# Performance work log

Measured on AMD Instinct MI355X. Metric: run time of the kernel, lower is better.

Reference implementation:

```python
import jax, jax.numpy as jnp
from jax import lax
import numpy as np

DG = 8          # deformable_groups
NF = 64         # num_feat
K = 3
KK = K * K


def conv3(x, w, b):
    # 3x3 'same' conv, NCHW / OIHW
    return lax.conv_general_dilated(x, w, (1, 1), 'SAME',
                                    dimension_numbers=('NCHW', 'OIHW', 'NCHW')) + b[None, :, None, None]


def deform_conv(x, offset, w, b, dg=DG):
    # Offset-only deformable conv (DCN), 3x3, stride 1, pad 1.
    # x: (B,C,H,W); offset: (B, dg*KK*2, H, W) ordered (group, kernel_pos, [dy,dx])
    B, C, H, W = x.shape
    Cg = C // dg
    dt = x.dtype
    off = offset.reshape(B, dg, KK, 2, H, W)
    gy = jnp.arange(H, dtype=dt)[:, None]                      # (H,1)
    gx = jnp.arange(W, dtype=dt)[None, :]                      # (1,W)
    ky = (jnp.arange(KK) // K - 1).astype(dt)[:, None, None]   # (KK,1,1)
    kx = (jnp.arange(KK) % K - 1).astype(dt)[:, None, None]
    py = gy + ky + off[:, :, :, 0]                             # (B,dg,KK,H,W)
    px = gx + kx + off[:, :, :, 1]
    xg = x.reshape(B, dg, Cg, H, W)

    def sample(img, py, px):
        # img (Cg,H,W); py,px (KK,H,W) -> (Cg,KK,H,W); zero padding outside image
        y0 = jnp.floor(py); x0 = jnp.floor(px)
        wy = py - y0; wx = px - x0
        y0 = y0.astype(jnp.int32); x0 = x0.astype(jnp.int32)
        imf = img.reshape(Cg, H * W)

        def gather(yi, xi):
            valid = ((yi >= 0) & (yi < H) & (xi >= 0) & (xi < W)).astype(dt)
            flat = (jnp.clip(yi, 0, H - 1) * W + jnp.clip(xi, 0, W - 1)).reshape(-1)
            return imf[:, flat].reshape(Cg, KK, H, W) * valid

        v00 = gather(y0, x0);     v01 = gather(y0, x0 + 1)
        v10 = gather(y0 + 1, x0); v11 = gather(y0 + 1, x0 + 1)
        return (v00 * (1 - wy) * (1 - wx) + v01 * (1 - wy) * wx
                + v10 * wy * (1 - wx) + v11 * wy * wx)

    samp = jax.vmap(jax.vmap(sample))(xg, py, px)   # (B,dg,Cg,KK,H,W)
    wr = w.reshape(-1, dg, Cg, KK)                  # (Cout,dg,Cg,KK) from (Cout,Cin,3,3)
    out = jnp.einsum('bgckhw,ogck->bohw', samp, wr)
    return out + b[None, :, None, None]


def _forward(pf, xc, cr_w, cr_b, off1_w, off1_b, dc1_w, dc1_b, off2_w, off2_b,
             dc2_w, dc2_b, off3_w, off3_b, dc3_w, dc3_b, off4_w, off4_b,
             dc4_w, dc4_b, rec_w, rec_b):
    B, N, C, H, W = pf.shape
    center = N // 2
    ref = pf[:, center]
    ys = []
    for i in range(N):  # N is a small static frame count (5)
        if i == center:
            ys.append(xc[:, None])
            continue
        supp = pf[:, i]
        fea = conv3(jnp.concatenate([ref, supp], axis=1), cr_w, cr_b)
        fea = deform_conv(fea, conv3(fea, off1_w, off1_b), dc1_w, dc1_b)
        fea = deform_conv(fea, conv3(fea, off2_w, off2_b), dc2_w, dc2_b)
        fea = deform_conv(supp, conv3(fea, off3_w, off3_b), dc3_w, dc3_b)
        aligned = deform_conv(fea, conv3(fea, off4_w, off4_b), dc4_w, dc4_b)
        ys.append(conv3(aligned, rec_w, rec_b)[:, None])
    return jnp.concatenate(ys, axis=1)  # (B, N, 3, H, W)


def setup_inputs() -> dict:
    key = jax.random.key(0)
    ks = jax.random.split(key, 16)
    B, N, C, H, W = 2, 5, NF, 128, 128
    offc = 18 * DG

    def cw(k, cout, cin):
        # matches init_weights: normal(0, sqrt(2 / (k*k*out_channels)))
        return jax.random.normal(k, (cout, cin, 3, 3), jnp.float32) * float(np.sqrt(2.0 / (9 * cout)))

    return {
        'precomputed_features': jax.random.normal(ks[0], (B, N, C, H, W), jnp.float32),
        'x_center': jax.random.normal(ks[1], (B, 3, H, W), jnp.float32),
        'cr_w': cw(ks[2], C, 2 * C), 'cr_b': jnp.zeros((C,), jnp.float32),
        'off1_w': cw(ks[3], offc, C), 'off1_b': jnp.zeros((offc,), jnp.float32),
        'dc1_w': cw(ks[4], C, C), 'dc1_b': jnp.zeros((C,), jnp.float32),
        'off2_w': cw(ks[5], offc, C), 'off2_b': jnp.zeros((offc,), jnp.float32),
        'dc2_w': cw(ks[6], C, C), 'dc2_b': jnp.zeros((C,), jnp.float32),
        'off3_w': cw(ks[7], offc, C), 'off3_b': jnp.zeros((offc,), jnp.float32),
        'dc3_w': cw(ks[8], C, C), 'dc3_b': jnp.zeros((C,), jnp.float32),
        'off4_w': cw(ks[9], offc, C), 'off4_b': jnp.zeros((offc,), jnp.float32),
        'dc4_w': cw(ks[10], C, C), 'dc4_b': jnp.zeros((C,), jnp.float32),
        'rec_w': cw(ks[11], 3, C), 'rec_b': jnp.zeros((3,), jnp.float32),
    }


def reference(precomputed_features, x_center, cr_w, cr_b, off1_w, off1_b, dc1_w, dc1_b,
              off2_w, off2_b, dc2_w, dc2_b, off3_w, off3_b, dc3_w, dc3_b,
              off4_w, off4_b, dc4_w, dc4_b, rec_w, rec_b):
    return _forward(precomputed_features, x_center, cr_w, cr_b, off1_w, off1_b, dc1_w, dc1_b,
                    off2_w, off2_b, dc2_w, dc2_b, off3_w, off3_b, dc3_w, dc3_b,
                    off4_w, off4_b, dc4_w, dc4_b, rec_w, rec_b)
```

## Files before the change

kernel.cpp:

```cpp
#include <hip/hip_runtime.h>

#define HH 128
#define WW 128
#define HWP (HH*WW)
#define NC 64
#define NB 2
#define NN 5
#define OFFC 144
#define NKC 18

typedef __attribute__((ext_vector_type(8))) _Float16 half8;
typedef __attribute__((ext_vector_type(4))) float floatx4;
typedef __attribute__((ext_vector_type(2))) float floatx2;

__global__ __launch_bounds__(256) void copy_center_k(const float* __restrict__ xc,
                                                     float* __restrict__ out) {
    int idx = blockIdx.x * 256 + threadIdx.x;
    const int total = NB * 3 * HWP;
    if (idx >= total) return;
    int b = idx / (3 * HWP);
    int r = idx - b * 3 * HWP;
    out[(size_t)((b * NN + 2) * 3) * HWP + r] = xc[idx];
}

__global__ __launch_bounds__(256) void repack_k(const float* __restrict__ pf,
                                                float* __restrict__ dst, int job0, int is_ref)
{
    __shared__ float T[64][65];
    const int jl = blockIdx.y;
    const float* src;
    if (is_ref) {
        src = pf + (size_t)((jl * NN + 2) * NC) * HWP;
    } else {
        int jg = job0 + jl;
        int b = jg & 1, fi = jg >> 1;
        int frame = fi + (fi >= 2 ? 1 : 0);
        src = pf + (size_t)((b * NN + frame) * NC) * HWP;
    }
    float* d = dst + (size_t)jl * NC * HWP;
    const int p0 = blockIdx.x * 64;
    const int tid = threadIdx.x;
    const int lx = tid & 63, cg4 = tid >> 6;
#pragma unroll
    for (int cc = 0; cc < 16; ++cc) {
        int c = cc * 4 + cg4;
        T[c][lx] = src[(size_t)c * HWP + p0 + lx];
    }
    __syncthreads();
    const int px = tid >> 2, c0 = (tid & 3) * 16;
#pragma unroll
    for (int j = 0; j < 4; ++j) {
        floatx4 v = { T[c0 + j*4 + 0][px], T[c0 + j*4 + 1][px],
                      T[c0 + j*4 + 2][px], T[c0 + j*4 + 3][px] };
        *(floatx4*)(d + (size_t)(p0 + px) * 64 + c0 + j*4) = v;
    }
}

__global__ __launch_bounds__(256) void prew_k(const float* __restrict__ w,
                                              _Float16* __restrict__ wp,
                                              int nct, int nkc, int mode,
                                              int ci_off, int cin_src)
{
    int idx = blockIdx.x * 256 + threadIdx.x;
    if (idx >= nct * nkc * 64) return;
    int lane = idx & 63;
    int kc = (idx >> 6) % nkc;
    int ct = (idx >> 6) / nkc;
    int m = lane & 15, quad = lane >> 4;
    int co = ct * 16 + m;
    union { half8 v; _Float16 e[8]; } ph, pl;
#pragma unroll
    for (int j = 0; j < 8; ++j) {
        int k = kc * 32 + quad * 8 + j;
        float f = 0.f;
        if (mode == 0) {
            int kk = k >> 6, ci = k & 63;
            f = w[((size_t)co * cin_src + ci_off + ci) * 9 + kk];
        } else {
            int r = k / 160, kr = k - r * 160;
            if (kr < 144) {
                int g = r * 2 + kr / 72;
                int rr = kr % 72;
                int kk = rr >> 3, cg = rr & 7;
                f = w[((size_t)co * cin_src + g * 8 + cg) * 9 + kk];
            }
        }
        _Float16 h = (_Float16)f;
        ph.e[j] = h; pl.e[j] = (_Float16)(f - (float)h);
    }
    size_t base = (size_t)((ct * nkc + kc) * 2) * 512;
    *(half8*)(wp + base + lane * 8) = ph.v;
    *(half8*)(wp + base + 512 + lane * 8) = pl.v;
}

template<int NCT, int SRCMODE, int ADD>
__global__ __launch_bounds__(256, 3) void mconv_k(
    const float* __restrict__ src, const float* __restrict__ R,
    const float* __restrict__ S, const _Float16* __restrict__ wp,
    const float* __restrict__ bias, float* __restrict__ out, int job0)
{
    constexpr int PL = 1456;
    constexpr int Ct = NCT * 16;
    const int jl = blockIdx.y, jg = job0 + jl;
    const int b = jg & 1;
    const int tile = blockIdx.x;
    const int ty0 = (tile >> 3) << 3, tx0 = (tile & 7) << 4;
    const int tid = threadIdx.x;
    const int lane = tid & 63;
    const int wq = __builtin_amdgcn_readfirstlane(tid >> 6);
    const int n = lane & 15, quad = lane >> 4;

    const float* s0;
    if (SRCMODE == 0)      s0 = src + (size_t)jl * NC * HWP;
    else if (SRCMODE == 1) s0 = R + (size_t)b * NC * HWP;
    else                   s0 = S + (size_t)jl * NC * HWP;

    __shared__ _Float16 hh[8 * PL];
    __shared__ _Float16 ll[8 * PL];

    for (int t = tid; t < 360; t += 256) {
        int px = t >> 1, hf = t & 1;
        int hy = px / 18, hx = px - hy * 18;
        int gy = ty0 - 1 + hy, gx = tx0 - 1 + hx;
        bool ok = (gy >= 0 && gy < HH && gx >= 0 && gx < WW);
        const float* sp = s0 + (ok ? ((size_t)(gy * WW + gx) * 64) : 0) + hf * 32;
        int lb = px * 8;
#pragma unroll
        for (int c = 0; c < 4; ++c) {
            int cb = hf * 4 + c;
            floatx4 f0 = {0.f,0.f,0.f,0.f}, f1 = {0.f,0.f,0.f,0.f};
            if (ok) {
                f0 = *(const floatx4*)(sp + c * 8);
                f1 = *(const floatx4*)(sp + c * 8 + 4);
            }
            union { half8 v; _Float16 e[8]; } ph, pl;
#pragma unroll
            for (int j = 0; j < 4; ++j) {
                _Float16 h0 = (_Float16)f0[j], h1 = (_Float16)f1[j];
                ph.e[j] = h0;     ph.e[j+4] = h1;
                pl.e[j] = (_Float16)(f0[j] - (float)h0);
                pl.e[j+4] = (_Float16)(f1[j] - (float)h1);
            }
            *(half8*)&hh[cb * PL + lb] = ph.v;
            *(half8*)&ll[cb * PL + lb] = pl.v;
        }
    }
    __syncthreads();

    floatx4 acc0[NCT], acc1[NCT];
#pragma unroll
    for (int ct = 0; ct < NCT; ++ct) {
        acc0[ct] = floatx4{0.f, 0.f, 0.f, 0.f};
        acc1[ct] = floatx4{0.f, 0.f, 0.f, 0.f};
    }
    const int y0 = wq * 2, y1 = y0 + 1;
#pragma unroll
    for (int kc = 0; kc < NKC; ++kc) {
        const int kk = kc >> 1;
        const int dy = kk / 3, dx = kk % 3;
        const int cb = ((kc & 1) << 2) + quad;
        const int ix0 = cb * PL + ((y0 + dy) * 18 + n + dx) * 8;
        const int ix1 = cb * PL + ((y1 + dy) * 18 + n + dx) * 8;
        half8 B0h = *(const half8*)&hh[ix0];
        half8 B0l = *(const half8*)&ll[ix0];
        half8 B1h = *(const half8*)&hh[ix1];
        half8 B1l = *(const half8*)&ll[ix1];
        const _Float16* wk = wp + (size_t)kc * 1024 + lane * 8;
#pragma unroll
        for (int ct = 0; ct < NCT; ++ct) {
            const _Float16* wc = wk + (size_t)ct * NKC * 1024;
            half8 Ah = *(const half8*)wc;
            half8 Al = *(const half8*)(wc + 512);
            acc0[ct] = __builtin_amdgcn_mfma_f32_16x16x32_f16(Ah, B0h, acc0[ct], 0, 0, 0);
            acc0[ct] = __builtin_amdgcn_mfma_f32_16x16x32_f16(Ah, B0l, acc0[ct], 0, 0, 0);
            acc0[ct] = __builtin_amdgcn_mfma_f32_16x16x32_f16(Al, B0h, acc0[ct], 0, 0, 0);
            acc1[ct] = __builtin_amdgcn_mfma_f32_16x16x32_f16(Ah, B1h, acc1[ct], 0, 0, 0);
            acc1[ct] = __builtin_amdgcn_mfma_f32_16x16x32_f16(Ah, B1l, acc1[ct], 0, 0, 0);
            acc1[ct] = __builtin_amdgcn_mfma_f32_16x16x32_f16(Al, B1h, acc1[ct], 0, 0, 0);
        }
    }

    const int oy0 = ty0 + y0, oy1 = ty0 + y1, ox = tx0 + n;
#pragma unroll
    for (int ct = 0; ct < NCT; ++ct) {
        const floatx4 b4 = *(const floatx4*)(bias + ct * 16 + quad * 4);
        float* op0 = out + ((size_t)jl * HWP + (size_t)oy0 * WW + ox) * Ct
                         + ct * 16 + quad * 4;
        float* op1 = out + ((size_t)jl * HWP + (size_t)oy1 * WW + ox) * Ct
                         + ct * 16 + quad * 4;
        floatx4 v0 = acc0[ct], v1 = acc1[ct];
        if (ADD) {
            v0 += *(const floatx4*)op0;
            v1 += *(const floatx4*)op1;
        } else {
            v0 += b4;
            v1 += b4;
        }
        *(floatx4*)op0 = v0;
        *(floatx4*)op1 = v1;
    }
}

__global__ __launch_bounds__(256, 4) void mdeform_k(
    const float* __restrict__ in, const float* __restrict__ off,
    const _Float16* __restrict__ wp, const float* __restrict__ bias,
    float* __restrict__ out, int supp_mode, const float* __restrict__ S)
{
    constexpr int SROW = 166;
    const int jl = blockIdx.y;
    const int tile = blockIdx.x;
    const int ty0 = (tile >> 4) << 3, tx0 = (tile & 15) << 3;
    const int tid = threadIdx.x;
    const int lane = tid & 63;
    const int q = __builtin_amdgcn_readfirstlane(tid >> 6);
    const int n = lane & 15, quad = lane >> 4;

    const float* ibase = supp_mode ? (S + (size_t)jl * NC * HWP)
                                   : (in + (size_t)jl * NC * HWP);
    const float* obase = off + (size_t)jl * OFFC * HWP;

    __shared__ _Float16 sh[64 * SROW];
    __shared__ _Float16 sl[64 * SROW];

    for (int e = tid; e < 64 * 16; e += 256) {
        int row = e >> 4, col = 144 + (e & 15);
        sh[row * SROW + col] = (_Float16)0.f;
        sl[row * SROW + col] = (_Float16)0.f;
    }

    floatx4 acc[4];
#pragma unroll
    for (int s = 0; s < 4; ++s) acc[s] = floatx4{0.f, 0.f, 0.f, 0.f};

    for (int r = 0; r < 4; ++r) {
        __syncthreads();
        for (int i = 0; i < 9; ++i) {
            int idx = tid + (i << 8);
            int hf = idx & 1;
            int pair = idx >> 1;
            int gl = pair / 576;
            int rem = pair - gl * 576;
            int kk = rem >> 6;
            int px = rem & 63;
            int g = r * 2 + gl;
            int yy = ty0 + (px >> 3), xx = tx0 + (px & 7);
            floatx2 o2 = *(const floatx2*)(obase + (size_t)(yy * WW + xx) * OFFC
                                           + (g * 9 + kk) * 2);
            float pyf = (float)(yy + (kk / 3) - 1) + o2[0];
            float pxf = (float)(xx + (kk % 3) - 1) + o2[1];
            float fy = floorf(pyf), fx = floorf(pxf);
            float wy = pyf - fy, wx = pxf - fx;
            int y0 = (int)fy, x0 = (int)fx;
            int y1 = y0 + 1, x1 = x0 + 1;
            float m00 = (y0 >= 0 && y0 < HH && x0 >= 0 && x0 < WW) ? 1.f : 0.f;
            float m01 = (y0 >= 0 && y0 < HH && x1 >= 0 && x1 < WW) ? 1.f : 0.f;
            float m10 = (y1 >= 0 && y1 < HH && x0 >= 0 && x0 < WW) ? 1.f : 0.f;
            float m11 = (y1 >= 0 && y1 < HH && x1 >= 0 && x1 < WW) ? 1.f : 0.f;
            float w00 = (1.f - wy) * (1.f - wx) * m00;
            float w01 = (1.f - wy) * wx * m01;
            float w10 = wy * (1.f - wx) * m10;
            float w11 = wy * wx * m11;
            int cy0 = min(max(y0, 0), HH - 1), cy1 = min(max(y1, 0), HH - 1);
            int cx0 = min(max(x0, 0), WW - 1), cx1 = min(max(x1, 0), WW - 1);
            const int co = g * 8 + hf * 4;
            const float* p00 = ibase + (size_t)(cy0 * WW + cx0) * 64 + co;
            const float* p01 = ibase + (size_t)(cy0 * WW + cx1) * 64 + co;
            const float* p10 = ibase + (size_t)(cy1 * WW + cx0) * 64 + co;
            const float* p11 = ibase + (size_t)(cy1 * WW + cx1) * 64 + co;
            floatx4 a = *(const floatx4*)p00;
            floatx4 b = *(const floatx4*)p01;
            floatx4 c = *(const floatx4*)p10;
            floatx4 d = *(const floatx4*)p11;
            floatx4 sv = a * w00 + b * w01 + c * w10 + d * w11;
            union { unsigned u[2]; _Float16 e[4]; } P, L;
#pragma unroll
            for (int j = 0; j < 4; ++j) {
                _Float16 h = (_Float16)sv[j];
                P.e[j] = h;
                L.e[j] = (_Float16)(sv[j] - (float)h);
            }
            int sb = px * SROW + gl * 72 + kk * 8 + hf * 4;
            unsigned* shp = (unsigned*)&sh[sb];
            unsigned* slp = (unsigned*)&sl[sb];
            shp[0] = P.u[0]; shp[1] = P.u[1];
            slp[0] = L.u[0]; slp[1] = L.u[1];
        }
        __syncthreads();
#pragma unroll
        for (int kc5 = 0; kc5 < 5; ++kc5) {
            int kcg = r * 5 + kc5;
            size_t base = (size_t)((q * 20 + kcg) * 2) * 512;
            half8 Ah = *(const half8*)(wp + base + lane * 8);
            half8 Al = *(const half8*)(wp + base + 512 + lane * 8);
#pragma unroll
            for (int s = 0; s < 4; ++s) {
                int px = s * 16 + n;
                const int ix = px * SROW + kc5 * 32 + quad * 8;
                half8 Bh = *(const half8*)&sh[ix];
                half8 Bl = *(const half8*)&sl[ix];
                acc[s] = __builtin_amdgcn_mfma_f32_16x16x32_f16(Ah, Bh, acc[s], 0, 0, 0);
                acc[s] = __builtin_amdgcn_mfma_f32_16x16x32_f16(Ah, Bl, acc[s], 0, 0, 0);
                acc[s] = __builtin_amdgcn_mfma_f32_16x16x32_f16(Al, Bh, acc[s], 0, 0, 0);
            }
        }
    }
    const floatx4 b4 = *(const floatx4*)(bias + q * 16 + quad * 4);
#pragma unroll
    for (int s = 0; s < 4; ++s) {
        int px = s * 16 + n;
        int oy = ty0 + (px >> 3), ox = tx0 + (px & 7);
        float* op = out + ((size_t)jl * HWP + (size_t)oy * WW + ox) * 64
                        + q * 16 + quad * 4;
        *(floatx4*)op = acc[s] + b4;
    }
}

__global__ __launch_bounds__(256) void conv3x3_rec_k(
    const float* __restrict__ in, const float* __restrict__ w,
    const float* __restrict__ bias, float* __restrict__ out, int job0)
{
    constexpr int CB = 8;
    constexpr int PITCH = 48;
    constexpr int CH = 18 * PITCH;
    const int jl = blockIdx.y, jg = job0 + jl;
    const int b = jg & 1, fi = jg >> 1;
    const int frame = fi + (fi >= 2 ? 1 : 0);
    const int tile = blockIdx.x;
    const int ty0 = (tile >> 3) << 4, tx0 = (tile & 7) << 4;
    const int tid = threadIdx.x;
    const int tx = tid & 15, ty = tid >> 4;
    const float* srcA = in + (size_t)jl * NC * HWP;

    __shared__ float lds[CB * CH];
    float acc[3] = {bias[0], bias[1], bias[2]};

    for (int cb = 0; cb < NC; cb += CB) {
        __syncthreads();
        for (int e = tid; e < CB * 324; e += 256) {
            int c = e & 7;
            int r = e >> 3;
            int iy = r / 18, ix = r - iy * 18;
            int gy = ty0 - 1 + iy, gx = tx0 - 1 + ix;
            float v = 0.f;
            if (gy >= 0 && gy < HH && gx >= 0 && gx < WW)
                v = srcA[(size_t)(gy * WW + gx) * 64 + cb + c];
            lds[c * CH + iy * PITCH + ix] = v;
        }
        __syncthreads();
#pragma unroll
        for (int c = 0; c < CB; ++c) {
            float t[9];
#pragma unroll
            for (int dy = 0; dy < 3; ++dy)
#pragma unroll
                for (int dx = 0; dx < 3; ++dx)
                    t[dy * 3 + dx] = lds[c * CH + (ty + dy) * PITCH + (tx + dx)];
            int ci = cb + c;
#pragma unroll
            for (int o = 0; o < 3; ++o) {
                const float* wo = w + ((size_t)o * NC + ci) * 9;
#pragma unroll
                for (int kk = 0; kk < 9; ++kk)
                    acc[o] = fmaf(wo[kk], t[kk], acc[o]);
            }
        }
    }
    const int oy = ty0 + ty, ox = tx0 + tx;
#pragma unroll
    for (int o = 0; o < 3; ++o)
        out[((size_t)(b * NN + frame) * 3 + o) * HWP + oy * WW + ox] = acc[o];
}

extern "C" void kernel_launch(void* const* d_in, const int* in_sizes, int n_in,
                              void* d_out, int out_size, void* d_ws, size_t ws_size,
                              hipStream_t stream)
{
    const float* pf    = (const float*)d_in[0];
    const float* xc    = (const float*)d_in[1];
    const float* cr_w  = (const float*)d_in[2];
    const float* cr_b  = (const float*)d_in[3];
    const float* ow[4] = {(const float*)d_in[4],  (const float*)d_in[8],
                          (const float*)d_in[12], (const float*)d_in[16]};
    const float* ob[4] = {(const float*)d_in[5],  (const float*)d_in[9],
                          (const float*)d_in[13], (const float*)d_in[17]};
    const float* dw[4] = {(const float*)d_in[6],  (const float*)d_in[10],
                          (const float*)d_in[14], (const float*)d_in[18]};
    const float* db[4] = {(const float*)d_in[7],  (const float*)d_in[11],
                          (const float*)d_in[15], (const float*)d_in[19]};
    const float* rec_w = (const float*)d_in[20];
    const float* rec_b = (const float*)d_in[21];
    float* out = (float*)d_out;

    const size_t WPC = (size_t)4 * NKC * 1024;
    const size_t WPO = (size_t)9 * NKC * 1024;
    const size_t WPD = (size_t)4 * 20 * 1024;
    _Float16* wp_cr0 = (_Float16*)d_ws;
    _Float16* wp_cr1 = wp_cr0 + WPC;
    _Float16* wp_of[4];
    _Float16* wp_dc[4];
    _Float16* curh = wp_cr1 + WPC;
    for (int i = 0; i < 4; ++i) { wp_of[i] = curh; curh += WPO; }
    for (int i = 0; i < 4; ++i) { wp_dc[i] = curh; curh += WPD; }
    size_t wp_bytes = (size_t)((char*)curh - (char*)d_ws);

    const size_t fplane = (size_t)NC * HWP;
    const size_t oplane = (size_t)OFFC * HWP;
    int JC = 8;
    while (JC > 1 &&
           wp_bytes + (2 + 3 * (size_t)JC) * fplane * 4 + (size_t)JC * oplane * 4 > ws_size)
        JC >>= 1;
    float* R  = (float*)curh;
    float* S  = R  + 2 * fplane;
    float* A  = S  + (size_t)JC * fplane;
    float* Bb = A  + (size_t)JC * fplane;
    float* O  = Bb + (size_t)JC * fplane;

    {
        int nc4 = 4 * NKC * 64, nc9 = 9 * NKC * 64, ncd = 4 * 20 * 64;
        dim3 b4((nc4 + 255) / 256), b9((nc9 + 255) / 256), bd((ncd + 255) / 256);
        prew_k<<<b4, 256, 0, stream>>>(cr_w, wp_cr0, 4, NKC, 0, 0, 128);
        prew_k<<<b4, 256, 0, stream>>>(cr_w, wp_cr1, 4, NKC, 0, 64, 128);
        for (int i = 0; i < 4; ++i) {
            prew_k<<<b9, 256, 0, stream>>>(ow[i], wp_of[i], 9, NKC, 0, 0, 64);
            prew_k<<<bd, 256, 0, stream>>>(dw[i], wp_dc[i], 4, 20, 1, 0, 64);
        }
        repack_k<<<dim3(256, 2), 256, 0, stream>>>(pf, R, 0, 1);
    }

    copy_center_k<<<dim3((NB * 3 * HWP + 255) / 256), 256, 0, stream>>>(xc, out);

    for (int job0 = 0; job0 < 8; job0 += JC) {
        dim3 blk(256);
        dim3 gconv(128, JC), gdef(256, JC), grec(64, JC);
        repack_k<<<dim3(256, JC), blk, 0, stream>>>(pf, S, job0, 0);
        mconv_k<4, 1, 0><<<gconv, blk, 0, stream>>>(nullptr, R, S, wp_cr0, cr_b, A, job0);
        mconv_k<4, 2, 1><<<gconv, blk, 0, stream>>>(nullptr, R, S, wp_cr1, cr_b, A, job0);
        mconv_k<9, 0, 0><<<gconv, blk, 0, stream>>>(A, R, S, wp_of[0], ob[0], O, job0);
        mdeform_k<<<gdef, blk, 0, stream>>>(A, O, wp_dc[0], db[0], Bb, 0, S);
        mconv_k<9, 0, 0><<<gconv, blk, 0, stream>>>(Bb, R, S, wp_of[1], ob[1], O, job0);
        mdeform_k<<<gdef, blk, 0, stream>>>(Bb, O, wp_dc[1], db[1], A, 0, S);
        mconv_k<9, 0, 0><<<gconv, blk, 0, stream>>>(A, R, S, wp_of[2], ob[2], O, job0);
        mdeform_k<<<gdef, blk, 0, stream>>>(nullptr, O, wp_dc[2], db[2], Bb, 1, S);
        mconv_k<9, 0, 0><<<gconv, blk, 0, stream>>>(Bb, R, S, wp_of[3], ob[3], O, job0);
        mdeform_k<<<gdef, blk, 0, stream>>>(Bb, O, wp_dc[3], db[3], A, 0, S);
        conv3x3_rec_k<<<grec, blk, 0, stream>>>(A, rec_w, rec_b, out, job0);
    }
}
```

Before: 1.326 ms.

## Process one deform group per round to shrink LDS and raise occupancy

The deformable conv kernel now stages one group (72 K-values padded to 96) per round over 8 rounds, where it used to stage two groups (144 padded to 160) over 4 rounds. The weight packing is changed to match the new K-chunk layout. This cuts shared memory per block from about 42KB to about 26KB, and launch bounds go from 4 to 6 blocks per CU for more latency hiding. In exchange there is more K padding (24 of 96 instead of 16 of 160), so more wasted MFMA work, and twice as many barriers.

```diff
diff --git a/kernel.cpp b/kernel.cpp
--- a/kernel.cpp
+++ b/kernel.cpp
@@ -8,6 +8,7 @@
 #define NN 5
 #define OFFC 144
 #define NKC 18
+#define DKC 24
 
 typedef __attribute__((ext_vector_type(8))) _Float16 half8;
 typedef __attribute__((ext_vector_type(4))) float floatx4;
@@ -77,12 +78,10 @@
             int kk = k >> 6, ci = k & 63;
             f = w[((size_t)co * cin_src + ci_off + ci) * 9 + kk];
         } else {
-            int r = k / 160, kr = k - r * 160;
-            if (kr < 144) {
-                int g = r * 2 + kr / 72;
-                int rr = kr % 72;
-                int kk = rr >> 3, cg = rr & 7;
-                f = w[((size_t)co * cin_src + g * 8 + cg) * 9 + kk];
+            int r = k / 96, kr = k - r * 96;
+            if (kr < 72) {
+                int kk = kr >> 3, cg = kr & 7;
+                f = w[((size_t)co * cin_src + r * 8 + cg) * 9 + kk];
             }
         }
         _Float16 h = (_Float16)f;
@@ -201,12 +200,12 @@
     }
 }
 
-__global__ __launch_bounds__(256, 4) void mdeform_k(
+__global__ __launch_bounds__(256, 6) void mdeform_k(
     const float* __restrict__ in, const float* __restrict__ off,
     const _Float16* __restrict__ wp, const float* __restrict__ bias,
     float* __restrict__ out, int supp_mode, const float* __restrict__ S)
 {
-    constexpr int SROW = 166;
+    constexpr int SROW = 102;
     const int jl = blockIdx.y;
     const int tile = blockIdx.x;
     const int ty0 = (tile >> 4) << 3, tx0 = (tile & 15) << 3;
@@ -222,8 +221,8 @@
     __shared__ _Float16 sh[64 * SROW];
     __shared__ _Float16 sl[64 * SROW];
 
-    for (int e = tid; e < 64 * 16; e += 256) {
-        int row = e >> 4, col = 144 + (e & 15);
+    for (int e = tid; e < 64 * 24; e += 256) {
+        int row = e / 24, col = 72 + (e % 24);
         sh[row * SROW + col] = (_Float16)0.f;
         sl[row * SROW + col] = (_Float16)0.f;
     }
@@ -232,20 +231,16 @@
 #pragma unroll
     for (int s = 0; s < 4; ++s) acc[s] = floatx4{0.f, 0.f, 0.f, 0.f};
 
-    for (int r = 0; r < 4; ++r) {
+    for (int r = 0; r < 8; ++r) {
         __syncthreads();
-        for (int i = 0; i < 9; ++i) {
-            int idx = tid + (i << 8);
-            int hf = idx & 1;
-            int pair = idx >> 1;
-            int gl = pair / 576;
-            int rem = pair - gl * 576;
-            int kk = rem >> 6;
-            int px = rem & 63;
-            int g = r * 2 + gl;
+        for (int tk = tid; tk < 1152; tk += 256) {
+            int hf = tk & 1;
+            int pair = tk >> 1;
+            int kk = pair >> 6;
+            int px = pair & 63;
             int yy = ty0 + (px >> 3), xx = tx0 + (px & 7);
             floatx2 o2 = *(const floatx2*)(obase + (size_t)(yy * WW + xx) * OFFC
-                                           + (g * 9 + kk) * 2);
+                                           + (r * 9 + kk) * 2);
             float pyf = (float)(yy + (kk / 3) - 1) + o2[0];
             float pxf = (float)(xx + (kk % 3) - 1) + o2[1];
             float fy = floorf(pyf), fx = floorf(pxf);
@@ -262,7 +257,7 @@
             float w11 = wy * wx * m11;
             int cy0 = min(max(y0, 0), HH - 1), cy1 = min(max(y1, 0), HH - 1);
             int cx0 = min(max(x0, 0), WW - 1), cx1 = min(max(x1, 0), WW - 1);
-            const int co = g * 8 + hf * 4;
+            const int co = r * 8 + hf * 4;
             const float* p00 = ibase + (size_t)(cy0 * WW + cx0) * 64 + co;
             const float* p01 = ibase + (size_t)(cy0 * WW + cx1) * 64 + co;
             const float* p10 = ibase + (size_t)(cy1 * WW + cx0) * 64 + co;
@@ -279,7 +274,7 @@
                 P.e[j] = h;
                 L.e[j] = (_Float16)(sv[j] - (float)h);
             }
-            int sb = px * SROW + gl * 72 + kk * 8 + hf * 4;
+            int sb = px * SROW + kk * 8 + hf * 4;
             unsigned* shp = (unsigned*)&sh[sb];
             unsigned* slp = (unsigned*)&sl[sb];
             shp[0] = P.u[0]; shp[1] = P.u[1];
@@ -287,15 +282,15 @@
         }
         __syncthreads();
 #pragma unroll
-        for (int kc5 = 0; kc5 < 5; ++kc5) {
-            int kcg = r * 5 + kc5;
-            size_t base = (size_t)((q * 20 + kcg) * 2) * 512;
+        for (int kc3 = 0; kc3 < 3; ++kc3) {
+            int kcg = r * 3 + kc3;
+            size_t base = (size_t)((q * DKC + kcg) * 2) * 512;
             half8 Ah = *(const half8*)(wp + base + lane * 8);
             half8 Al = *(const half8*)(wp + base + 512 + lane * 8);
 #pragma unroll
             for (int s = 0; s < 4; ++s) {
                 int px = s * 16 + n;
-                const int ix = px * SROW + kc5 * 32 + quad * 8;
+                const int ix = px * SROW + kc3 * 32 + quad * 8;
                 half8 Bh = *(const half8*)&sh[ix];
                 half8 Bl = *(const half8*)&sl[ix];
                 acc[s] = __builtin_amdgcn_mfma_f32_16x16x32_f16(Ah, Bh, acc[s], 0, 0, 0);
@@ -393,7 +388,7 @@
 
     const size_t WPC = (size_t)4 * NKC * 1024;
     const size_t WPO = (size_t)9 * NKC * 1024;
-    const size_t WPD = (size_t)4 * 20 * 1024;
+    const size_t WPD = (size_t)4 * DKC * 1024;
     _Float16* wp_cr0 = (_Float16*)d_ws;
     _Float16* wp_cr1 = wp_cr0 + WPC;
     _Float16* wp_of[4];
@@ -416,13 +411,13 @@
     float* O  = Bb + (size_t)JC * fplane;
 
     {
-        int nc4 = 4 * NKC * 64, nc9 = 9 * NKC * 64, ncd = 4 * 20 * 64;
+        int nc4 = 4 * NKC * 64, nc9 = 9 * NKC * 64, ncd = 4 * DKC * 64;
         dim3 b4((nc4 + 255) / 256), b9((nc9 + 255) / 256), bd((ncd + 255) / 256);
         prew_k<<<b4, 256, 0, stream>>>(cr_w, wp_cr0, 4, NKC, 0, 0, 128);
         prew_k<<<b4, 256, 0, stream>>>(cr_w, wp_cr1, 4, NKC, 0, 64, 128);
         for (int i = 0; i < 4; ++i) {
             prew_k<<<b9, 256, 0, stream>>>(ow[i], wp_of[i], 9, NKC, 0, 0, 64);
-            prew_k<<<bd, 256, 0, stream>>>(dw[i], wp_dc[i], 4, 20, 1, 0, 64);
+            prew_k<<<bd, 256, 0, stream>>>(dw[i], wp_dc[i], 4, DKC, 1, 0, 64);
         }
         repack_k<<<dim3(256, 2), 256, 0, stream>>>(pf, R, 0, 1);
     }
```

Result: slower. 1.446 ms (+9.0%).
